# Performance work log

Hardware: AMD Instinct MI355X
Metric: run time of the kernel (lower is better)

Reference implementation:

```python
import jax, jax.numpy as jnp
import numpy as np

N = 20000   # total nodes (all graphs flattened)
E = 640000  # total edges
D = 512     # num_node_features
H = 512     # hidden_channels
G = 64      # number of graphs in the batch


def setup_inputs() -> dict:
    key = jax.random.key(0)
    ks = jax.random.split(key, 12)
    s = 0.05
    return {
        "x_a": jax.random.normal(ks[0], (N, D), dtype=jnp.float32),
        "edge_index_a": jax.random.randint(ks[1], (2, E), 0, N),
        "batch_a": jnp.sort(jax.random.randint(ks[2], (N,), 0, G)),
        "x_b": jax.random.normal(ks[3], (N, D), dtype=jnp.float32),
        "edge_index_b": jax.random.randint(ks[4], (2, E), 0, N),
        "batch_b": jnp.sort(jax.random.randint(ks[5], (N,), 0, G)),
        "W1": jax.random.normal(ks[6], (D, H), dtype=jnp.float32) * s,
        "b1": jnp.zeros((H,), dtype=jnp.float32),
        "W2": jax.random.normal(ks[7], (H, H), dtype=jnp.float32) * s,
        "b2": jnp.zeros((H,), dtype=jnp.float32),
        "W3": jax.random.normal(ks[8], (H, H), dtype=jnp.float32) * s,
        "b3": jnp.zeros((H,), dtype=jnp.float32),
    }


def _gcn_conv(x, src, dst, W, b, n):
    # GCNConv with self-loops and symmetric normalization:
    # out = D^{-1/2} (A + I) D^{-1/2} X W + b,  deg_i = 1 + in_degree(i)
    h = x @ W                                                  # [n, H]
    deg = jax.ops.segment_sum(jnp.ones((src.shape[0],), h.dtype), dst,
                              num_segments=n) + 1.0            # self-loop
    dinv = jax.lax.rsqrt(deg)                                  # deg^{-1/2}
    norm = dinv[src] * dinv[dst]                               # [E]
    agg = jax.ops.segment_sum(h[src] * norm[:, None], dst, num_segments=n)
    agg = agg + h * (dinv * dinv)[:, None]                     # self-loop term
    return agg + b


def _encode(x, edge_index, batch, W1, b1, W2, b2, W3, b3):
    src, dst = edge_index[0], edge_index[1]
    n = x.shape[0]
    h = jax.nn.relu(_gcn_conv(x, src, dst, W1, b1, n))
    h = jax.nn.relu(_gcn_conv(h, src, dst, W2, b2, n))
    h = _gcn_conv(h, src, dst, W3, b3, n)
    # global mean pool over graphs
    sums = jax.ops.segment_sum(h, batch, num_segments=G)       # [G, H]
    cnts = jax.ops.segment_sum(jnp.ones((n,), h.dtype), batch, num_segments=G)
    return sums / jnp.maximum(cnts, 1.0)[:, None]


def reference(x_a, edge_index_a, batch_a, x_b, edge_index_b, batch_b,
              W1, b1, W2, b2, W3, b3):
    out_a = _encode(x_a, edge_index_a, batch_a, W1, b1, W2, b2, W3, b3)
    out_b = _encode(x_b, edge_index_b, batch_b, W1, b1, W2, b2, W3, b3)
    # torch F.pairwise_distance: ||a - b + eps||_2 with eps=1e-6
    return jnp.linalg.norm(out_a - out_b + 1e-6, axis=-1)      # [G]
```

## Files before the change

kernel.cpp:

```cpp
#include <hip/hip_runtime.h>
#include <hip/hip_fp16.h>


typedef short bf16x8 __attribute__((ext_vector_type(8)));
typedef float f32x4 __attribute__((ext_vector_type(4)));

__device__ __forceinline__ unsigned short f2bf(float f) {
    union { float f; unsigned u; } v; v.f = f;
    unsigned r = (v.u + 0x7fffu + ((v.u >> 16) & 1u)) >> 16;
    return (unsigned short)r;
}
__device__ __forceinline__ float bf2f(unsigned short h) {
    union { unsigned u; float f; } v; v.u = ((unsigned)h) << 16;
    return v.f;
}

__device__ __forceinline__ void gload16(const unsigned short* g, unsigned short* lds) {
    __builtin_amdgcn_global_load_lds(
        (const __attribute__((address_space(1))) unsigned int*)g,
        (__attribute__((address_space(3))) unsigned int*)lds, 16, 0, 0);
}


__global__ __launch_bounds__(256) void deg_kernel(const int* __restrict__ dst,
                                                  int* __restrict__ deg, int e) {
    int i = blockIdx.x * 256 + threadIdx.x;
    if (i < e) atomicAdd(&deg[dst[i]], 1);
}

__global__ __launch_bounds__(1024) void scan2_kernel(const int* __restrict__ deg_all,
                                                     int* __restrict__ rp_all,
                                                     int* __restrict__ cur_all,
                                                     float* __restrict__ dinv_all, int n) {
    int enc = blockIdx.x;
    const int* deg = deg_all + (size_t)enc * n;
    int* row_ptr = rp_all + (size_t)enc * (n + 1);
    int* cursor = cur_all + (size_t)enc * n;
    float* dinv = dinv_all + (size_t)enc * n;

    __shared__ int sums[1024];
    int t = threadIdx.x;
    int chunk = (n + 1023) >> 10;
    int beg = t * chunk;
    int end = beg + chunk;
    if (beg > n) beg = n;
    if (end > n) end = n;
    int s = 0;
    for (int i = beg; i < end; ++i) s += deg[i];
    sums[t] = s;
    __syncthreads();
    for (int off = 1; off < 1024; off <<= 1) {
        int v = (t >= off) ? sums[t - off] : 0;
        __syncthreads();
        sums[t] += v;
        __syncthreads();
    }
    int run = sums[t] - s;
    for (int i = beg; i < end; ++i) {
        row_ptr[i] = run;
        cursor[i] = run;
        dinv[i] = rsqrtf((float)deg[i] + 1.0f);
        run += deg[i];
    }
    if (t == 1023) row_ptr[n] = sums[1023];
}

__global__ __launch_bounds__(256) void fill_kernel(const int* __restrict__ src,
                                                   const int* __restrict__ dst,
                                                   const float* __restrict__ dinv,
                                                   int* __restrict__ cursor,
                                                   int2* __restrict__ edges, int e) {
    int i = blockIdx.x * 256 + threadIdx.x;
    if (i >= e) return;
    int s = src[i], d = dst[i];
    int p = atomicAdd(&cursor[d], 1);
    int2 pr;
    pr.x = s;
    pr.y = __float_as_int(dinv[s] * dinv[d]);
    edges[p] = pr;
}


__global__ __launch_bounds__(256) void ranges_kernel(const int* __restrict__ batch,
                                                     int* __restrict__ start, int n, int g) {
    int i = blockIdx.x * 256 + threadIdx.x;
    if (i >= n) return;
    int b = batch[i];
    if (i == 0) {
        for (int k = 0; k <= b; ++k) start[k] = 0;
    } else {
        int pb = batch[i - 1];
        for (int k = pb + 1; k <= b; ++k) start[k] = i;
    }
    if (i == n - 1) {
        for (int k = b + 1; k <= g; ++k) start[k] = n;
    }
}


__global__ __launch_bounds__(256) void wsplit_kernel(const float* __restrict__ W,
                                                     unsigned short* __restrict__ Wt_hi,
                                                     unsigned short* __restrict__ Wt_lo) {
    __shared__ float tile[32][33];
    int b = blockIdx.x;
    int k0 = (b & 15) * 32, n0 = (b >> 4) * 32;
    int t = threadIdx.x;
    int tc = t & 31, tr = t >> 5;
#pragma unroll
    for (int it = 0; it < 4; ++it)
        tile[tr + it * 8][tc] = W[(size_t)(k0 + tr + it * 8) * 512 + n0 + tc];
    __syncthreads();
#pragma unroll
    for (int it = 0; it < 4; ++it) {
        int n = tr + it * 8;
        float v = tile[tc][n];
        unsigned short hi = f2bf(v);
        unsigned short lo = f2bf(v - bf2f(hi));
        Wt_hi[(size_t)(n0 + n) * 512 + k0 + tc] = hi;
        Wt_lo[(size_t)(n0 + n) * 512 + k0 + tc] = lo;
    }
}


__global__ __launch_bounds__(256) void asplit_kernel(const float* __restrict__ A,
                                                     unsigned short* __restrict__ A_hi,
                                                     unsigned short* __restrict__ A_lo,
                                                     int n4) {
    int i = blockIdx.x * 256 + threadIdx.x;
    if (i >= n4) return;
    float4 v = ((const float4*)A)[i];
    ushort4 h, l;
    h.x = f2bf(v.x); l.x = f2bf(v.x - bf2f(h.x));
    h.y = f2bf(v.y); l.y = f2bf(v.y - bf2f(h.y));
    h.z = f2bf(v.z); l.z = f2bf(v.z - bf2f(h.z));
    h.w = f2bf(v.w); l.w = f2bf(v.w - bf2f(h.w));
    ((ushort4*)A_hi)[i] = h;
    ((ushort4*)A_lo)[i] = l;
}


__global__ __launch_bounds__(256) void gemm_mfma_kernel(const unsigned short* __restrict__ A_hi,
                                                        const unsigned short* __restrict__ A_lo,
                                                        const unsigned short* __restrict__ Bt_hi,
                                                        const unsigned short* __restrict__ Bt_lo,
                                                        __half* __restrict__ C, int M) {
    __shared__ unsigned short As_hi[128][32], As_lo[128][32];
    __shared__ unsigned short Bs_hi[128][32], Bs_lo[128][32];
    int nb = blockIdx.x & 3;
    int mb = blockIdx.x >> 2;
    int row0 = mb * 128, col0 = nb * 128;
    int t = threadIdx.x;
    int lane = t & 63, w = t >> 6;
    int wm = w >> 1, wn = w & 1;
    int r = lane & 15, g = lane >> 4;

    f32x4 acc[4][4] = {};

    int r4 = t >> 2;
    int kq = (t & 3) * 8;

    for (int k0 = 0; k0 < 512; k0 += 32) {
#pragma unroll
        for (int i = 0; i < 2; ++i) {
            int ldsrow = i * 64 + w * 16;
            gload16(A_hi + (size_t)(row0 + i * 64 + r4) * 512 + k0 + kq, &As_hi[ldsrow][0]);
            gload16(A_lo + (size_t)(row0 + i * 64 + r4) * 512 + k0 + kq, &As_lo[ldsrow][0]);
            gload16(Bt_hi + (size_t)(col0 + i * 64 + r4) * 512 + k0 + kq, &Bs_hi[ldsrow][0]);
            gload16(Bt_lo + (size_t)(col0 + i * 64 + r4) * 512 + k0 + kq, &Bs_lo[ldsrow][0]);
        }
        __syncthreads();

        bf16x8 ah[4], al[4], bh[4], bl[4];
#pragma unroll
        for (int m = 0; m < 4; ++m) {
            int rr = wm * 64 + m * 16 + r;
            ah[m] = *(const bf16x8*)&As_hi[rr][g * 8];
            al[m] = *(const bf16x8*)&As_lo[rr][g * 8];
        }
#pragma unroll
        for (int n = 0; n < 4; ++n) {
            int cc = wn * 64 + n * 16 + r;
            bh[n] = *(const bf16x8*)&Bs_hi[cc][g * 8];
            bl[n] = *(const bf16x8*)&Bs_lo[cc][g * 8];
        }
#pragma unroll
        for (int m = 0; m < 4; ++m)
#pragma unroll
            for (int n = 0; n < 4; ++n) {
                acc[m][n] = __builtin_amdgcn_mfma_f32_16x16x32_bf16(al[m], bh[n], acc[m][n], 0, 0, 0);
                acc[m][n] = __builtin_amdgcn_mfma_f32_16x16x32_bf16(ah[m], bl[n], acc[m][n], 0, 0, 0);
                acc[m][n] = __builtin_amdgcn_mfma_f32_16x16x32_bf16(ah[m], bh[n], acc[m][n], 0, 0, 0);
            }
        __syncthreads();
    }

#pragma unroll
    for (int m = 0; m < 4; ++m)
#pragma unroll
        for (int j = 0; j < 4; ++j) {
            int rr = row0 + wm * 64 + m * 16 + g * 4 + j;
            if (rr < M) {
#pragma unroll
                for (int n = 0; n < 4; ++n)
                    C[(size_t)rr * 512 + col0 + wn * 64 + n * 16 + r] =
                        __float2half(acc[m][n][j]);
            }
        }
}


template <bool RELU, bool SPLIT>
__global__ __launch_bounds__(256) void aggregate_kernel(const __half* __restrict__ H,
                                                        const int* __restrict__ rp_all,
                                                        const int2* __restrict__ ed_all,
                                                        const float* __restrict__ dinv_all,
                                                        const float* __restrict__ bias,
                                                        float* __restrict__ X,
                                                        unsigned short* __restrict__ Xhi,
                                                        unsigned short* __restrict__ Xlo,
                                                        int n, int e) {
    int dg = blockIdx.x;
    bool isB = dg >= n;
    int d = isB ? dg - n : dg;
    const int* rp = rp_all + (isB ? (size_t)(n + 1) : 0);
    const int2* ed = ed_all + (isB ? (size_t)e : 0);
    const float* dv = dinv_all + (isB ? (size_t)n : 0);
    const __half* Hb = H + (isB ? (size_t)n * 512 : 0);

    int t = threadIdx.x;
    int beg = rp[d], end = rp[d + 1];
    float ax = 0.f, ay = 0.f;
    int j = beg;
    for (; j + 4 <= end; j += 4) {
        int2 e0 = ed[j], e1 = ed[j + 1], e2 = ed[j + 2], e3 = ed[j + 3];
        __half2 h0 = *(const __half2*)(Hb + (size_t)e0.x * 512 + t * 2);
        __half2 h1 = *(const __half2*)(Hb + (size_t)e1.x * 512 + t * 2);
        __half2 h2 = *(const __half2*)(Hb + (size_t)e2.x * 512 + t * 2);
        __half2 h3 = *(const __half2*)(Hb + (size_t)e3.x * 512 + t * 2);
        float2 f0 = __half22float2(h0), f1 = __half22float2(h1);
        float2 f2 = __half22float2(h2), f3 = __half22float2(h3);
        float w0 = __int_as_float(e0.y), w1 = __int_as_float(e1.y);
        float w2 = __int_as_float(e2.y), w3 = __int_as_float(e3.y);
        ax += w0 * f0.x + w1 * f1.x + w2 * f2.x + w3 * f3.x;
        ay += w0 * f0.y + w1 * f1.y + w2 * f2.y + w3 * f3.y;
    }
    for (; j < end; ++j) {
        int2 ej = ed[j];
        float w = __int_as_float(ej.y);
        float2 f = __half22float2(*(const __half2*)(Hb + (size_t)ej.x * 512 + t * 2));
        ax += w * f.x;
        ay += w * f.y;
    }
    float di = dv[d];
    float self = di * di;
    float2 hd = __half22float2(*(const __half2*)(Hb + (size_t)d * 512 + t * 2));
    float2 bb = *(const float2*)(bias + t * 2);
    float ox = ax + self * hd.x + bb.x;
    float oy = ay + self * hd.y + bb.y;
    if (RELU) {
        ox = fmaxf(ox, 0.f);
        oy = fmaxf(oy, 0.f);
    }
    if (SPLIT) {
        unsigned short hx = f2bf(ox), hy = f2bf(oy);
        unsigned short lx = f2bf(ox - bf2f(hx)), ly = f2bf(oy - bf2f(hy));
        *(ushort2*)(Xhi + (size_t)dg * 512 + t * 2) = make_ushort2(hx, hy);
        *(ushort2*)(Xlo + (size_t)dg * 512 + t * 2) = make_ushort2(lx, ly);
    } else {
        *(float2*)(X + (size_t)dg * 512 + t * 2) = make_float2(ox, oy);
    }
}


__global__ __launch_bounds__(256) void pool_kernel(const float* __restrict__ X,
                                                   const int* __restrict__ startA,
                                                   const int* __restrict__ startB,
                                                   float* __restrict__ pool,
                                                   int n, int gcount) {
    int g = blockIdx.x;
    bool isB = g >= gcount;
    const int* st = isB ? startB : startA;
    int gl = isB ? g - gcount : g;
    const float* Xb = X + (isB ? (size_t)n * 512 : 0);
    int t = threadIdx.x;
    int s = st[gl], e = st[gl + 1];
    float ax = 0.f, ay = 0.f;
    int i = s;
    for (; i + 2 <= e; i += 2) {
        float2 v0 = *(const float2*)(Xb + (size_t)i * 512 + t * 2);
        float2 v1 = *(const float2*)(Xb + (size_t)(i + 1) * 512 + t * 2);
        ax += v0.x + v1.x;
        ay += v0.y + v1.y;
    }
    for (; i < e; ++i) {
        float2 v = *(const float2*)(Xb + (size_t)i * 512 + t * 2);
        ax += v.x;
        ay += v.y;
    }
    float cnt = fmaxf((float)(e - s), 1.0f);
    *(float2*)(pool + (size_t)g * 512 + t * 2) = make_float2(ax / cnt, ay / cnt);
}


__global__ __launch_bounds__(64) void pdist_kernel(const float* __restrict__ pool,
                                                   float* __restrict__ out, int gcount) {
    int g = blockIdx.x;
    int t = threadIdx.x;
    const float* pa = pool + (size_t)g * 512;
    const float* pb = pool + (size_t)(gcount + g) * 512;
    float s = 0.f;
    for (int i = t; i < 512; i += 64) {
        float d = pa[i] - pb[i] + 1e-6f;
        s += d * d;
    }
#pragma unroll
    for (int off = 32; off; off >>= 1) s += __shfl_down(s, off);
    if (t == 0) out[g] = sqrtf(s);
}


extern "C" void kernel_launch(void* const* d_in, const int* in_sizes, int n_in,
                              void* d_out, int out_size, void* d_ws, size_t ws_size,
                              hipStream_t stream) {
    const float* x_a = (const float*)d_in[0];
    const int* ei_a = (const int*)d_in[1];
    const int* batch_a = (const int*)d_in[2];
    const float* x_b = (const float*)d_in[3];
    const int* ei_b = (const int*)d_in[4];
    const int* batch_b = (const int*)d_in[5];
    const float* W1 = (const float*)d_in[6];
    const float* b1 = (const float*)d_in[7];
    const float* W2 = (const float*)d_in[8];
    const float* b2 = (const float*)d_in[9];
    const float* W3 = (const float*)d_in[10];
    const float* b3 = (const float*)d_in[11];
    float* out = (float*)d_out;

    const int N = in_sizes[0] / 512;
    const int E = in_sizes[1] / 2;
    const int G = out_size;
    const int M = 2 * N;
    const int Mpad = ((M + 127) / 128) * 128;

    char* ws = (char*)d_ws;
    size_t off = 0;
    auto alloc = [&](size_t bytes) -> void* {
        void* p = ws + off;
        off = (off + bytes + 255) & ~(size_t)255;
        return p;
    };
    __half* bufH16 = (__half*)alloc((size_t)Mpad * 512 * 2);
    char* abblock = (char*)alloc((size_t)Mpad * 512 * 4);
    unsigned short* a_hi = (unsigned short*)abblock;
    unsigned short* a_lo = a_hi + (size_t)Mpad * 512;
    float* bufX = (float*)abblock;
    int* deg = (int*)alloc((size_t)2 * N * 4);
    float* dinv = (float*)alloc((size_t)2 * N * 4);
    int* rp = (int*)alloc((size_t)2 * (N + 1) * 4);
    int* cur = (int*)alloc((size_t)2 * N * 4);
    int2* ed = (int2*)alloc((size_t)2 * E * 8);
    int* startA = (int*)alloc((size_t)(G + 1) * 4);
    int* startB = (int*)alloc((size_t)(G + 1) * 4);
    float* pool = (float*)alloc((size_t)2 * G * 512 * 4);
    unsigned short* wt_hi[3];
    unsigned short* wt_lo[3];
    for (int i = 0; i < 3; ++i) {
        wt_hi[i] = (unsigned short*)alloc((size_t)512 * 512 * 2);
        wt_lo[i] = (unsigned short*)alloc((size_t)512 * 512 * 2);
    }

    const int ebl = (E + 255) / 256;
    const int nbl = (N + 255) / 256;
    const int gemm_grid = 4 * (Mpad / 128);
    const int n4 = N * 512 / 4;
    const int abl = (n4 + 255) / 256;

    wsplit_kernel<<<256, 256, 0, stream>>>(W1, wt_hi[0], wt_lo[0]);
    wsplit_kernel<<<256, 256, 0, stream>>>(W2, wt_hi[1], wt_lo[1]);
    wsplit_kernel<<<256, 256, 0, stream>>>(W3, wt_hi[2], wt_lo[2]);

    hipMemsetAsync(deg, 0, (size_t)2 * N * 4, stream);
    deg_kernel<<<ebl, 256, 0, stream>>>(ei_a + E, deg, E);
    deg_kernel<<<ebl, 256, 0, stream>>>(ei_b + E, deg + N, E);
    scan2_kernel<<<2, 1024, 0, stream>>>(deg, rp, cur, dinv, N);
    fill_kernel<<<ebl, 256, 0, stream>>>(ei_a, ei_a + E, dinv, cur, ed, E);
    fill_kernel<<<ebl, 256, 0, stream>>>(ei_b, ei_b + E, dinv + N, cur + N, ed + E, E);
    ranges_kernel<<<nbl, 256, 0, stream>>>(batch_a, startA, N, G);
    ranges_kernel<<<nbl, 256, 0, stream>>>(batch_b, startB, N, G);

    asplit_kernel<<<abl, 256, 0, stream>>>(x_a, a_hi, a_lo, n4);
    asplit_kernel<<<abl, 256, 0, stream>>>(x_b, a_hi + (size_t)N * 512, a_lo + (size_t)N * 512, n4);

    gemm_mfma_kernel<<<gemm_grid, 256, 0, stream>>>(a_hi, a_lo, wt_hi[0], wt_lo[0], bufH16, M);
    aggregate_kernel<true, true><<<M, 256, 0, stream>>>(bufH16, rp, ed, dinv, b1,
                                                        bufX, a_hi, a_lo, N, E);
    gemm_mfma_kernel<<<gemm_grid, 256, 0, stream>>>(a_hi, a_lo, wt_hi[1], wt_lo[1], bufH16, M);
    aggregate_kernel<true, true><<<M, 256, 0, stream>>>(bufH16, rp, ed, dinv, b2,
                                                        bufX, a_hi, a_lo, N, E);
    gemm_mfma_kernel<<<gemm_grid, 256, 0, stream>>>(a_hi, a_lo, wt_hi[2], wt_lo[2], bufH16, M);
    aggregate_kernel<false, false><<<M, 256, 0, stream>>>(bufH16, rp, ed, dinv, b3,
                                                          bufX, a_hi, a_lo, N, E);

    pool_kernel<<<2 * G, 256, 0, stream>>>(bufX, startA, startB, pool, N, G);
    pdist_kernel<<<G, 64, 0, stream>>>(pool, out, G);
}
```

Measured before the change: 1.109 ms.

## Double-buffer GEMM LDS staging and merge per-encoder setup kernels

The MFMA GEMM now double-buffers its LDS tiles, issuing the async global-to-LDS load for the next k-slice before computing on the current one, with one barrier per iteration. Launch bounds now request two blocks per CU. Paired setup kernels (degree count, CSR fill, batch ranges, input split, and the three weight splits) are each merged into one launch covering both encoders or all layers. This aims to hide global load latency in the GEMM and cut launch overhead, at the cost of twice the GEMM shared memory and some register pressure from the occupancy hint.

```diff
diff --git a/kernel.cpp b/kernel.cpp
--- a/kernel.cpp
+++ b/kernel.cpp
@@ -22,10 +22,17 @@
 }
 
 
-__global__ __launch_bounds__(256) void deg_kernel(const int* __restrict__ dst,
-                                                  int* __restrict__ deg, int e) {
+__global__ __launch_bounds__(256) void deg2_kernel(const int* __restrict__ ei_a,
+                                                   const int* __restrict__ ei_b,
+                                                   int* __restrict__ deg,
+                                                   int n, int e) {
     int i = blockIdx.x * 256 + threadIdx.x;
-    if (i < e) atomicAdd(&deg[dst[i]], 1);
+    if (i >= 2 * e) return;
+    if (i < e) {
+        atomicAdd(&deg[ei_a[e + i]], 1);
+    } else {
+        atomicAdd(&deg[n + ei_b[e + (i - e)]], 1);
+    }
 }
 
 __global__ __launch_bounds__(1024) void scan2_kernel(const int* __restrict__ deg_all,
@@ -65,14 +72,21 @@
     if (t == 1023) row_ptr[n] = sums[1023];
 }
 
-__global__ __launch_bounds__(256) void fill_kernel(const int* __restrict__ src,
-                                                   const int* __restrict__ dst,
-                                                   const float* __restrict__ dinv,
-                                                   int* __restrict__ cursor,
-                                                   int2* __restrict__ edges, int e) {
+__global__ __launch_bounds__(256) void fill2_kernel(const int* __restrict__ ei_a,
+                                                    const int* __restrict__ ei_b,
+                                                    const float* __restrict__ dinv_all,
+                                                    int* __restrict__ cur_all,
+                                                    int2* __restrict__ ed_all,
+                                                    int n, int e) {
     int i = blockIdx.x * 256 + threadIdx.x;
-    if (i >= e) return;
-    int s = src[i], d = dst[i];
+    if (i >= 2 * e) return;
+    int enc = (i >= e) ? 1 : 0;
+    int j = i - enc * e;
+    const int* ei = enc ? ei_b : ei_a;
+    const float* dinv = dinv_all + (size_t)enc * n;
+    int* cursor = cur_all + (size_t)enc * n;
+    int2* edges = ed_all + (size_t)enc * e;
+    int s = ei[j], d = ei[e + j];
     int p = atomicAdd(&cursor[d], 1);
     int2 pr;
     pr.x = s;
@@ -81,28 +95,41 @@
 }
 
 
-__global__ __launch_bounds__(256) void ranges_kernel(const int* __restrict__ batch,
-                                                     int* __restrict__ start, int n, int g) {
+__global__ __launch_bounds__(256) void ranges2_kernel(const int* __restrict__ batch_a,
+                                                      const int* __restrict__ batch_b,
+                                                      int* __restrict__ startA,
+                                                      int* __restrict__ startB,
+                                                      int n, int g) {
     int i = blockIdx.x * 256 + threadIdx.x;
-    if (i >= n) return;
-    int b = batch[i];
-    if (i == 0) {
+    if (i >= 2 * n) return;
+    int enc = (i >= n) ? 1 : 0;
+    int j = i - enc * n;
+    const int* batch = enc ? batch_b : batch_a;
+    int* start = enc ? startB : startA;
+    int b = batch[j];
+    if (j == 0) {
         for (int k = 0; k <= b; ++k) start[k] = 0;
     } else {
-        int pb = batch[i - 1];
-        for (int k = pb + 1; k <= b; ++k) start[k] = i;
-    }
-    if (i == n - 1) {
+        int pb = batch[j - 1];
+        for (int k = pb + 1; k <= b; ++k) start[k] = j;
+    }
+    if (j == n - 1) {
         for (int k = b + 1; k <= g; ++k) start[k] = n;
     }
 }
 
 
-__global__ __launch_bounds__(256) void wsplit_kernel(const float* __restrict__ W,
-                                                     unsigned short* __restrict__ Wt_hi,
-                                                     unsigned short* __restrict__ Wt_lo) {
+__global__ __launch_bounds__(256) void wsplit3_kernel(const float* __restrict__ W1,
+                                                      const float* __restrict__ W2,
+                                                      const float* __restrict__ W3,
+                                                      unsigned short* __restrict__ hi_all,
+                                                      unsigned short* __restrict__ lo_all) {
     __shared__ float tile[32][33];
-    int b = blockIdx.x;
+    int layer = blockIdx.x >> 8;
+    int b = blockIdx.x & 255;
+    const float* W = (layer == 0) ? W1 : (layer == 1) ? W2 : W3;
+    unsigned short* Wt_hi = hi_all + (size_t)layer * 512 * 512;
+    unsigned short* Wt_lo = lo_all + (size_t)layer * 512 * 512;
     int k0 = (b & 15) * 32, n0 = (b >> 4) * 32;
     int t = threadIdx.x;
     int tc = t & 31, tr = t >> 5;
@@ -122,13 +149,14 @@
 }
 
 
-__global__ __launch_bounds__(256) void asplit_kernel(const float* __restrict__ A,
-                                                     unsigned short* __restrict__ A_hi,
-                                                     unsigned short* __restrict__ A_lo,
-                                                     int n4) {
+__global__ __launch_bounds__(256) void asplit2_kernel(const float* __restrict__ x_a,
+                                                      const float* __restrict__ x_b,
+                                                      unsigned short* __restrict__ A_hi,
+                                                      unsigned short* __restrict__ A_lo,
+                                                      int n4) {
     int i = blockIdx.x * 256 + threadIdx.x;
-    if (i >= n4) return;
-    float4 v = ((const float4*)A)[i];
+    if (i >= 2 * n4) return;
+    float4 v = (i < n4) ? ((const float4*)x_a)[i] : ((const float4*)x_b)[i - n4];
     ushort4 h, l;
     h.x = f2bf(v.x); l.x = f2bf(v.x - bf2f(h.x));
     h.y = f2bf(v.y); l.y = f2bf(v.y - bf2f(h.y));
@@ -139,13 +167,13 @@
 }
 
 
-__global__ __launch_bounds__(256) void gemm_mfma_kernel(const unsigned short* __restrict__ A_hi,
-                                                        const unsigned short* __restrict__ A_lo,
-                                                        const unsigned short* __restrict__ Bt_hi,
-                                                        const unsigned short* __restrict__ Bt_lo,
-                                                        __half* __restrict__ C, int M) {
-    __shared__ unsigned short As_hi[128][32], As_lo[128][32];
-    __shared__ unsigned short Bs_hi[128][32], Bs_lo[128][32];
+__global__ __launch_bounds__(256, 2) void gemm_mfma_kernel(const unsigned short* __restrict__ A_hi,
+                                                           const unsigned short* __restrict__ A_lo,
+                                                           const unsigned short* __restrict__ Bt_hi,
+                                                           const unsigned short* __restrict__ Bt_lo,
+                                                           __half* __restrict__ C, int M) {
+    __shared__ unsigned short As_hi[2][128][32], As_lo[2][128][32];
+    __shared__ unsigned short Bs_hi[2][128][32], Bs_lo[2][128][32];
     int nb = blockIdx.x & 3;
     int mb = blockIdx.x >> 2;
     int row0 = mb * 128, col0 = nb * 128;
@@ -159,29 +187,36 @@
     int r4 = t >> 2;
     int kq = (t & 3) * 8;
 
-    for (int k0 = 0; k0 < 512; k0 += 32) {
+    auto STAGE = [&](int buf, int k0) {
 #pragma unroll
         for (int i = 0; i < 2; ++i) {
             int ldsrow = i * 64 + w * 16;
-            gload16(A_hi + (size_t)(row0 + i * 64 + r4) * 512 + k0 + kq, &As_hi[ldsrow][0]);
-            gload16(A_lo + (size_t)(row0 + i * 64 + r4) * 512 + k0 + kq, &As_lo[ldsrow][0]);
-            gload16(Bt_hi + (size_t)(col0 + i * 64 + r4) * 512 + k0 + kq, &Bs_hi[ldsrow][0]);
-            gload16(Bt_lo + (size_t)(col0 + i * 64 + r4) * 512 + k0 + kq, &Bs_lo[ldsrow][0]);
+            gload16(A_hi + (size_t)(row0 + i * 64 + r4) * 512 + k0 + kq, &As_hi[buf][ldsrow][0]);
+            gload16(A_lo + (size_t)(row0 + i * 64 + r4) * 512 + k0 + kq, &As_lo[buf][ldsrow][0]);
+            gload16(Bt_hi + (size_t)(col0 + i * 64 + r4) * 512 + k0 + kq, &Bs_hi[buf][ldsrow][0]);
+            gload16(Bt_lo + (size_t)(col0 + i * 64 + r4) * 512 + k0 + kq, &Bs_lo[buf][ldsrow][0]);
         }
-        __syncthreads();
+    };
+
+    STAGE(0, 0);
+    __syncthreads();
+
+    int cur = 0;
+    for (int ks = 0; ks < 16; ++ks) {
+        if (ks < 15) STAGE(cur ^ 1, (ks + 1) * 32);
 
         bf16x8 ah[4], al[4], bh[4], bl[4];
 #pragma unroll
         for (int m = 0; m < 4; ++m) {
             int rr = wm * 64 + m * 16 + r;
-            ah[m] = *(const bf16x8*)&As_hi[rr][g * 8];
-            al[m] = *(const bf16x8*)&As_lo[rr][g * 8];
+            ah[m] = *(const bf16x8*)&As_hi[cur][rr][g * 8];
+            al[m] = *(const bf16x8*)&As_lo[cur][rr][g * 8];
         }
 #pragma unroll
         for (int n = 0; n < 4; ++n) {
             int cc = wn * 64 + n * 16 + r;
-            bh[n] = *(const bf16x8*)&Bs_hi[cc][g * 8];
-            bl[n] = *(const bf16x8*)&Bs_lo[cc][g * 8];
+            bh[n] = *(const bf16x8*)&Bs_hi[cur][cc][g * 8];
+            bl[n] = *(const bf16x8*)&Bs_lo[cur][cc][g * 8];
         }
 #pragma unroll
         for (int m = 0; m < 4; ++m)
@@ -192,6 +227,7 @@
                 acc[m][n] = __builtin_amdgcn_mfma_f32_16x16x32_bf16(ah[m], bh[n], acc[m][n], 0, 0, 0);
             }
         __syncthreads();
+        cur ^= 1;
     }
 
 #pragma unroll
@@ -362,42 +398,31 @@
     int* startA = (int*)alloc((size_t)(G + 1) * 4);
     int* startB = (int*)alloc((size_t)(G + 1) * 4);
     float* pool = (float*)alloc((size_t)2 * G * 512 * 4);
-    unsigned short* wt_hi[3];
-    unsigned short* wt_lo[3];
-    for (int i = 0; i < 3; ++i) {
-        wt_hi[i] = (unsigned short*)alloc((size_t)512 * 512 * 2);
-        wt_lo[i] = (unsigned short*)alloc((size_t)512 * 512 * 2);
-    }
-
-    const int ebl = (E + 255) / 256;
-    const int nbl = (N + 255) / 256;
+    unsigned short* wt_hi = (unsigned short*)alloc((size_t)3 * 512 * 512 * 2);
+    unsigned short* wt_lo = (unsigned short*)alloc((size_t)3 * 512 * 512 * 2);
+
     const int gemm_grid = 4 * (Mpad / 128);
     const int n4 = N * 512 / 4;
-    const int abl = (n4 + 255) / 256;
-
-    wsplit_kernel<<<256, 256, 0, stream>>>(W1, wt_hi[0], wt_lo[0]);
-    wsplit_kernel<<<256, 256, 0, stream>>>(W2, wt_hi[1], wt_lo[1]);
-    wsplit_kernel<<<256, 256, 0, stream>>>(W3, wt_hi[2], wt_lo[2]);
+
+    wsplit3_kernel<<<768, 256, 0, stream>>>(W1, W2, W3, wt_hi, wt_lo);
 
     hipMemsetAsync(deg, 0, (size_t)2 * N * 4, stream);
-    deg_kernel<<<ebl, 256, 0, stream>>>(ei_a + E, deg, E);
-    deg_kernel<<<ebl, 256, 0, stream>>>(ei_b + E, deg + N, E);
+    deg2_kernel<<<(2 * E + 255) / 256, 256, 0, stream>>>(ei_a, ei_b, deg, N, E);
     scan2_kernel<<<2, 1024, 0, stream>>>(deg, rp, cur, dinv, N);
-    fill_kernel<<<ebl, 256, 0, stream>>>(ei_a, ei_a + E, dinv, cur, ed, E);
-    fill_kernel<<<ebl, 256, 0, stream>>>(ei_b, ei_b + E, dinv + N, cur + N, ed + E, E);
-    ranges_kernel<<<nbl, 256, 0, stream>>>(batch_a, startA, N, G);
-    ranges_kernel<<<nbl, 256, 0, stream>>>(batch_b, startB, N, G);
-
-    asplit_kernel<<<abl, 256, 0, stream>>>(x_a, a_hi, a_lo, n4);
-    asplit_kernel<<<abl, 256, 0, stream>>>(x_b, a_hi + (size_t)N * 512, a_lo + (size_t)N * 512, n4);
-
-    gemm_mfma_kernel<<<gemm_grid, 256, 0, stream>>>(a_hi, a_lo, wt_hi[0], wt_lo[0], bufH16, M);
+    fill2_kernel<<<(2 * E + 255) / 256, 256, 0, stream>>>(ei_a, ei_b, dinv, cur, ed, N, E);
+    ranges2_kernel<<<(2 * N + 255) / 256, 256, 0, stream>>>(batch_a, batch_b, startA, startB, N, G);
+
+    asplit2_kernel<<<(2 * n4 + 255) / 256, 256, 0, stream>>>(x_a, x_b, a_hi, a_lo, n4);
+
+    gemm_mfma_kernel<<<gemm_grid, 256, 0, stream>>>(a_hi, a_lo, wt_hi, wt_lo, bufH16, M);
     aggregate_kernel<true, true><<<M, 256, 0, stream>>>(bufH16, rp, ed, dinv, b1,
                                                         bufX, a_hi, a_lo, N, E);
-    gemm_mfma_kernel<<<gemm_grid, 256, 0, stream>>>(a_hi, a_lo, wt_hi[1], wt_lo[1], bufH16, M);
+    gemm_mfma_kernel<<<gemm_grid, 256, 0, stream>>>(a_hi, a_lo, wt_hi + (size_t)512 * 512,
+                                                    wt_lo + (size_t)512 * 512, bufH16, M);
     aggregate_kernel<true, true><<<M, 256, 0, stream>>>(bufH16, rp, ed, dinv, b2,
                                                         bufX, a_hi, a_lo, N, E);
-    gemm_mfma_kernel<<<gemm_grid, 256, 0, stream>>>(a_hi, a_lo, wt_hi[2], wt_lo[2], bufH16, M);
+    gemm_mfma_kernel<<<gemm_grid, 256, 0, stream>>>(a_hi, a_lo, wt_hi + (size_t)2 * 512 * 512,
+                                                    wt_lo + (size_t)2 * 512 * 512, bufH16, M);
     aggregate_kernel<false, false><<<M, 256, 0, stream>>>(bufH16, rp, ed, dinv, b3,
                                                           bufX, a_hi, a_lo, N, E);
 
```

New measurement: 1.116 ms. Within noise of the previous version (+0.6%).
